# Kernel optimization log

Hardware: AMD Instinct MI355X
Metric: run time of the kernel (lower is better)

## Reference

```python
import jax, jax.numpy as jnp
import numpy as np

B, L, D, H = 4, 2048, 1024, 16
HD = D // H  # head_dim = 64


def setup_inputs() -> dict:
    key = jax.random.key(0)
    k1, k2, k3, k4 = jax.random.split(key, 4)
    x = jax.random.normal(k1, (B, L, D), dtype=jnp.float32)
    key_padding_mask = jax.random.randint(k2, (B, L), 0, 2) == 1
    scale = 1.0 / np.sqrt(D)
    Wqkv = jax.random.normal(k3, (3 * D, D), dtype=jnp.float32) * scale
    Wproj = jax.random.normal(k4, (D, D), dtype=jnp.float32) * scale
    return {"x": x, "key_padding_mask": key_padding_mask, "Wqkv": Wqkv, "Wproj": Wproj}


def reference(x, key_padding_mask, Wqkv, Wproj):
    b, l, d = x.shape
    qkv = jnp.einsum('bld,ed->ble', x, Wqkv)          # [B, L, 3D]
    q, k, v = jnp.split(qkv, 3, axis=-1)
    # [B, H, L, HD]
    q = q.reshape(b, l, H, HD).transpose(0, 2, 1, 3)
    k = k.reshape(b, l, H, HD).transpose(0, 2, 1, 3)
    v = v.reshape(b, l, H, HD).transpose(0, 2, 1, 3)
    scale = 1.0 / jnp.sqrt(jnp.asarray(HD, dtype=x.dtype))
    scores = jnp.einsum('bhqd,bhkd->bhqk', q, k) * scale  # [B, H, L, L]
    # key_padding_mask True = PAD -> -inf bias on key axis
    bias = jnp.where(key_padding_mask[:, None, None, :], -jnp.inf, 0.0).astype(x.dtype)
    attn = jax.nn.softmax(scores + bias, axis=-1)
    y = jnp.einsum('bhqk,bhkd->bhqd', attn, v)            # [B, H, L, HD]
    y = y.transpose(0, 2, 1, 3).reshape(b, l, d)          # [B, L, D]
    return jnp.einsum('bld,ed->ble', y, Wproj)
```

## Files before the change

kernel.cpp:

```cpp
#include <hip/hip_runtime.h>

#define L_SEQ 2048
#define DIM   1024
#define NH    16
#define HDIM  64
#define KDIM  1024

typedef short  short8 __attribute__((ext_vector_type(8)));
typedef __bf16 bf16x8 __attribute__((ext_vector_type(8)));
typedef __bf16 bf16x4 __attribute__((ext_vector_type(4)));
typedef float  f32x4  __attribute__((ext_vector_type(4)));
typedef unsigned u32x4 __attribute__((ext_vector_type(4)));

__device__ __forceinline__ unsigned short f2bf(float f) {
  unsigned u = __builtin_bit_cast(unsigned, f);
  u += 0x7fffu + ((u >> 16) & 1u);
  return (unsigned short)(u >> 16);
}

__device__ __forceinline__ void gload16(const void* g, void* l) {
  __builtin_amdgcn_global_load_lds(
      (const __attribute__((address_space(1))) void*)g,
      (__attribute__((address_space(3))) void*)l, 16, 0, 0);
}

__device__ __forceinline__ bf16x8 ldfrag(const unsigned short* p) {
  return __builtin_bit_cast(bf16x8, *(const short8*)p);
}
#define MFMA16(a, b, c) __builtin_amdgcn_mfma_f32_16x16x32_bf16(a, b, c, 0, 0, 0)

__device__ __forceinline__ unsigned cvtpk(float a, float b) {
  unsigned r;
  asm("v_cvt_pk_bf16_f32 %0, %1, %2" : "=v"(r) : "v"(a), "v"(b));
  return r;
}
__device__ __forceinline__ void xchg(unsigned &a, unsigned &b) {
  asm("v_permlane32_swap_b32 %0, %1" : "+v"(a), "+v"(b));
  asm("v_permlane16_swap_b32 %0, %1" : "+v"(a), "+v"(b));
}

__device__ __forceinline__ float foldmax_g(float v) {
  float y;
  asm("v_mov_b32 %0, %1" : "=&v"(y) : "v"(v));
  asm("v_permlane32_swap_b32 %0, %1" : "+v"(v), "+v"(y));
  v = fmaxf(v, y);
  float z;
  asm("v_mov_b32 %0, %1" : "=&v"(z) : "v"(v));
  asm("v_permlane16_swap_b32 %0, %1" : "+v"(v), "+v"(z));
  return fmaxf(v, z);
}

__device__ __forceinline__ void cvt_chunk(const float* __restrict__ src,
                                          unsigned short* __restrict__ dst,
                                          int blk, int t) {
  int i = (blk * 256 + t) * 8;
  f32x4 a = *(const f32x4*)(src + i);
  f32x4 b = *(const f32x4*)(src + i + 4);
  short8 o;
  o[0] = (short)f2bf(a[0]); o[1] = (short)f2bf(a[1]);
  o[2] = (short)f2bf(a[2]); o[3] = (short)f2bf(a[3]);
  o[4] = (short)f2bf(b[0]); o[5] = (short)f2bf(b[1]);
  o[6] = (short)f2bf(b[2]); o[7] = (short)f2bf(b[3]);
  *(short8*)(dst + i) = o;
}

__global__ __launch_bounds__(256) void prep(
    const float* __restrict__ x, const float* __restrict__ wqkv,
    const float* __restrict__ wproj, const int* __restrict__ mask,
    unsigned short* __restrict__ xb, unsigned short* __restrict__ wqkvb,
    unsigned short* __restrict__ wprojb,
    int* __restrict__ rowl, int* __restrict__ lc) {
  const int bid = blockIdx.x, t = threadIdx.x;
  if (bid < 4096)      { cvt_chunk(x,     xb,     bid,        t); return; }
  if (bid < 5632)      { cvt_chunk(wqkv,  wqkvb,  bid - 4096, t); return; }
  if (bid < 6144)      { cvt_chunk(wproj, wprojb, bid - 5632, t); return; }
  const int b = bid - 6144;
  __shared__ int wsum[4];
  __shared__ int lcs;
  const int* mrow = mask + b * L_SEQ + t * 8;
  int m[8], c = 0;
#pragma unroll
  for (int i = 0; i < 8; ++i) { m[i] = mrow[i]; c += (m[i] == 0); }
  const int lane = t & 63, w = t >> 6;
  int sc = c;
#pragma unroll
  for (int d = 1; d < 64; d <<= 1) {
    int v = __shfl_up(sc, d);
    if (lane >= d) sc += v;
  }
  if (lane == 63) wsum[w] = sc;
  __syncthreads();
  int pre = sc - c;
  for (int i = 0; i < w; ++i) pre += wsum[i];
  int run = pre;
#pragma unroll
  for (int i = 0; i < 8; ++i) {
    if (m[i] == 0) { rowl[b * L_SEQ + run] = t * 8 + i; ++run; }
  }
  if (t == 255) { lc[b] = run; lcs = run; }
  __syncthreads();
  int total = lcs;
#pragma unroll
  for (int i = 0; i < 8; ++i) {
    int slot = t * 8 + i;
    if (slot >= total) rowl[b * L_SEQ + slot] = 0;
  }
}

__device__ __forceinline__ void gemm512_mainloop(
    const unsigned short* __restrict__ A, const unsigned short* __restrict__ Bt,
    const int (&asrc)[2], int n0,
    unsigned short* As0, unsigned short* As1,
    unsigned short* Bs0, unsigned short* Bs1,
    f32x4 (&acc)[4][2]) {
  const int t = threadIdx.x;
  const int lane = t & 63, wid = t >> 6;
  const int wm = wid >> 2, wn = wid & 3;
  const int lr = lane & 15, lk = (lane >> 4) * 8;
  const int swr = (lr & 7) << 3;
  constexpr int NT = KDIM / 64;

  auto stage = [&](unsigned short* Ad, unsigned short* Bd, int kt) {
#pragma unroll
    for (int i = 0; i < 2; ++i) {
      int c = i * 512 + t;
      int row = c >> 3;
      int cs = ((c & 7) ^ (row & 7)) * 8;
      gload16(A + (size_t)asrc[i] * KDIM + kt * 64 + cs,
              Ad + row * 64 + (c & 7) * 8);
    }
#pragma unroll
    for (int i = 0; i < 2; ++i) {
      int c = i * 512 + t;
      int row = c >> 3;
      int cs = ((c & 7) ^ (row & 7)) * 8;
      gload16(Bt + (size_t)(n0 + row) * KDIM + kt * 64 + cs,
              Bd + row * 64 + (c & 7) * 8);
    }
  };

  auto tile = [&](const unsigned short* Ac, const unsigned short* Bc,
                  unsigned short* An, unsigned short* Bn, int kt) {
    if (kt + 1 < NT) {
      stage(An, Bn, kt + 1);
      asm volatile("s_waitcnt vmcnt(4)" ::: "memory");
    } else {
      asm volatile("s_waitcnt vmcnt(0)" ::: "memory");
    }
    __builtin_amdgcn_sched_barrier(0);
    __builtin_amdgcn_s_barrier();
    __builtin_amdgcn_sched_barrier(0);
    bf16x8 af[4][2], bfv[2][2];
#pragma unroll
    for (int mf = 0; mf < 4; ++mf)
#pragma unroll
      for (int kh = 0; kh < 2; ++kh)
        af[mf][kh] = ldfrag(Ac + (wm * 64 + mf * 16 + lr) * 64 +
                            ((kh * 32 + lk) ^ swr));
#pragma unroll
    for (int nf = 0; nf < 2; ++nf)
#pragma unroll
      for (int kh = 0; kh < 2; ++kh)
        bfv[nf][kh] = ldfrag(Bc + (wn * 32 + nf * 16 + lr) * 64 +
                             ((kh * 32 + lk) ^ swr));
    __builtin_amdgcn_s_setprio(1);
#pragma unroll
    for (int mf = 0; mf < 4; ++mf)
#pragma unroll
      for (int nf = 0; nf < 2; ++nf) {
        acc[mf][nf] = MFMA16(af[mf][0], bfv[nf][0], acc[mf][nf]);
        acc[mf][nf] = MFMA16(af[mf][1], bfv[nf][1], acc[mf][nf]);
      }
    __builtin_amdgcn_s_setprio(0);
    __builtin_amdgcn_sched_barrier(0);
    __builtin_amdgcn_s_barrier();
  };

  stage(As0, Bs0, 0);
  for (int kt = 0; kt < NT; kt += 2) {
    tile(As0, Bs0, As1, Bs1, kt);
    tile(As1, Bs1, As0, Bs0, kt + 1);
  }
}

__global__ __launch_bounds__(512, 4) void gemm_qkv(
    const unsigned short* __restrict__ xb, const unsigned short* __restrict__ wb,
    const int* __restrict__ rowl, const int* __restrict__ lc,
    unsigned short* __restrict__ qw, unsigned short* __restrict__ kw,
    unsigned short* __restrict__ vtw) {
  __shared__ unsigned short As[2][128 * 64];
  __shared__ unsigned short Bs[2][128 * 64];
  const int nx = blockIdx.x;
  const int m0 = blockIdx.y * 128;
  const int sec = nx >> 3;
  const int n0 = nx * 128;
  const int b = m0 >> 11;
  const int lcb = lc[b];
  if (sec > 0 && (m0 & 2047) >= lcb) return;
  const int t = threadIdx.x;
  int asrc[2];
#pragma unroll
  for (int i = 0; i < 2; ++i) {
    int p = m0 + i * 64 + (t >> 3);
    asrc[i] = (sec == 0) ? p : ((p & ~2047) + rowl[p]);
  }
  f32x4 acc[4][2] = {};
  gemm512_mainloop(xb, wb, asrc, n0, As[0], As[1], Bs[0], Bs[1], acc);

  const int lane = t & 63, wid = t >> 6;
  const int wm = wid >> 2, wn = wid & 3;
  const int lr = lane & 15, g4 = (lane >> 4) * 4;
  const int nb = n0 & 1023;
  if (sec == 0) {
#pragma unroll
    for (int mf = 0; mf < 4; ++mf)
#pragma unroll
      for (int nf = 0; nf < 2; ++nf) {
        int e2 = nb + wn * 32 + nf * 16 + lr;
        int h = e2 >> 6, hd = e2 & 63;
#pragma unroll
        for (int r = 0; r < 4; ++r) {
          int m = m0 + wm * 64 + mf * 16 + g4 + r;
          qw[(((size_t)(b * NH + h)) * L_SEQ + (m & 2047)) * HDIM + hd] =
              f2bf(acc[mf][nf][r]);
        }
      }
  } else {
#pragma unroll
    for (int mf = 0; mf < 4; ++mf)
#pragma unroll
      for (int r = 0; r < 4; ++r) {
        int m = m0 + wm * 64 + mf * 16 + g4 + r;
        int tgt = m & 2047;
        size_t bb = (size_t)b * NH;
        if (sec == 1) {
          if (tgt >= lcb) continue;
#pragma unroll
          for (int nf = 0; nf < 2; ++nf) {
            int e2 = nb + wn * 32 + nf * 16 + lr;
            int h = e2 >> 6, hd = e2 & 63;
            kw[((bb + h) * L_SEQ + tgt) * HDIM + hd] = f2bf(acc[mf][nf][r]);
          }
        } else {
#pragma unroll
          for (int nf = 0; nf < 2; ++nf) {
            int e2 = nb + wn * 32 + nf * 16 + lr;
            int h = e2 >> 6, hd = e2 & 63;
            unsigned short val = (tgt < lcb) ? f2bf(acc[mf][nf][r])
                                             : (unsigned short)0;
            vtw[((bb + h) * HDIM + hd) * L_SEQ + tgt] = val;
          }
        }
      }
  }
}

__global__ __launch_bounds__(512, 4) void gemm_proj(
    const unsigned short* __restrict__ yb, const unsigned short* __restrict__ wb,
    float* __restrict__ out) {
  __shared__ unsigned short As[2][128 * 64];
  __shared__ unsigned short Bs[2][128 * 64];
  const int n0 = blockIdx.x * 128, m0 = blockIdx.y * 128;
  const int t = threadIdx.x;
  int asrc[2];
#pragma unroll
  for (int i = 0; i < 2; ++i) asrc[i] = m0 + i * 64 + (t >> 3);
  f32x4 acc[4][2] = {};
  gemm512_mainloop(yb, wb, asrc, n0, As[0], As[1], Bs[0], Bs[1], acc);
  const int lane = t & 63, wid = t >> 6;
  const int wm = wid >> 2, wn = wid & 3;
  const int lr = lane & 15, g4 = (lane >> 4) * 4;
#pragma unroll
  for (int mf = 0; mf < 4; ++mf)
#pragma unroll
    for (int nf = 0; nf < 2; ++nf) {
      int e2 = n0 + wn * 32 + nf * 16 + lr;
#pragma unroll
      for (int r = 0; r < 4; ++r) {
        int m = m0 + wm * 64 + mf * 16 + g4 + r;
        out[(size_t)m * DIM + e2] = acc[mf][nf][r];
      }
    }
}

__global__ __launch_bounds__(256, 4) void attn_kernel(
    const unsigned short* __restrict__ qw, const unsigned short* __restrict__ kw,
    const unsigned short* __restrict__ vtw, const int* __restrict__ lc,
    unsigned short* __restrict__ yb) {
  __shared__ unsigned short Ks[2][64 * 64];
  __shared__ unsigned short Vts[2][64 * 64];
  const int bh = blockIdx.y;
  const int q0 = blockIdx.x * 128;
  const int b = bh >> 4, h = bh & 15;
  const int t = threadIdx.x, wid = t >> 6, lane = t & 63;
  const int lr = lane & 15, lk = (lane >> 4) * 8, g4 = (lane >> 4) * 4;
  const int swr = (lr & 7) << 3;
  const float KE = 0.18033688011112042f;

  const int Lcv = lc[b];
  const int nt = (Lcv + 63) >> 6;

  bf16x8 qf[2][2];
  const size_t qbase = (size_t)bh * L_SEQ + q0 + wid * 32;
#pragma unroll
  for (int qi = 0; qi < 2; ++qi)
#pragma unroll
    for (int kh = 0; kh < 2; ++kh)
      qf[qi][kh] = __builtin_bit_cast(bf16x8,
          *(const short8*)(qw + (qbase + qi * 16 + lr) * HDIM + kh * 32 + lk));

  f32x4 o[2][4] = {};
  float mrun[2] = {-3.0e38f, -3.0e38f};
  float lrun[2] = {0.f, 0.f};

  auto stage = [&](int buf, int kt) {
#pragma unroll
    for (int i = 0; i < 2; ++i) {
      int c = i * 256 + t;
      int row = c >> 3;
      int cs = ((c & 7) ^ (row & 7)) * 8;
      gload16(kw  + ((size_t)bh * L_SEQ + kt * 64 + row) * HDIM + cs, &Ks[buf][c * 8]);
      gload16(vtw + ((size_t)bh * HDIM + row) * L_SEQ + kt * 64 + cs, &Vts[buf][c * 8]);
    }
  };

  stage(0, 0);
  int cur = 0;

  for (int kt = 0; kt < nt; ++kt) {
    if (kt + 1 < nt) {
      stage(cur ^ 1, kt + 1);
      asm volatile("s_waitcnt vmcnt(4)" ::: "memory");
    } else {
      asm volatile("s_waitcnt vmcnt(0)" ::: "memory");
    }
    __builtin_amdgcn_s_barrier();
    __builtin_amdgcn_sched_barrier(0);

    const unsigned short* Kc = Ks[cur];
    f32x4 s[2][4] = {};
    __builtin_amdgcn_s_setprio(1);
#pragma unroll
    for (int nf = 0; nf < 4; ++nf) {
      bf16x8 k0 = __builtin_bit_cast(bf16x8,
          *(const short8*)(Kc + (nf * 16 + lr) * 64 + ((0 + lk) ^ swr)));
      bf16x8 k1 = __builtin_bit_cast(bf16x8,
          *(const short8*)(Kc + (nf * 16 + lr) * 64 + ((32 + lk) ^ swr)));
      s[0][nf] = MFMA16(k0, qf[0][0], s[0][nf]);
      s[0][nf] = MFMA16(k1, qf[0][1], s[0][nf]);
      s[1][nf] = MFMA16(k0, qf[1][0], s[1][nf]);
      s[1][nf] = MFMA16(k1, qf[1][1], s[1][nf]);
    }
    __builtin_amdgcn_s_setprio(0);

    if (kt == nt - 1) {
      int kbase = kt * 64 + g4;
#pragma unroll
      for (int nf = 0; nf < 4; ++nf)
#pragma unroll
        for (int r = 0; r < 4; ++r)
          if (kbase + nf * 16 + r >= Lcv) {
            s[0][nf][r] = -3.0e38f;
            s[1][nf][r] = -3.0e38f;
          }
    }

    float pmax[2];
#pragma unroll
    for (int qi = 0; qi < 2; ++qi) {
      float a0 = fmaxf(fmaxf(s[qi][0][0], s[qi][0][1]), fmaxf(s[qi][0][2], s[qi][0][3]));
      float a1 = fmaxf(fmaxf(s[qi][1][0], s[qi][1][1]), fmaxf(s[qi][1][2], s[qi][1][3]));
      float a2 = fmaxf(fmaxf(s[qi][2][0], s[qi][2][1]), fmaxf(s[qi][2][2], s[qi][2][3]));
      float a3 = fmaxf(fmaxf(s[qi][3][0], s[qi][3][1]), fmaxf(s[qi][3][2], s[qi][3][3]));
      pmax[qi] = foldmax_g(fmaxf(fmaxf(a0, a1), fmaxf(a2, a3)));
    }

    bool need = (pmax[0] > mrun[0] + 8.0f) || (pmax[1] > mrun[1] + 8.0f);
    if (__any(need)) {
#pragma unroll
      for (int qi = 0; qi < 2; ++qi) {
        float mn = fmaxf(mrun[qi], pmax[qi]);
        float al = __builtin_amdgcn_exp2f((mrun[qi] - mn) * KE);
        mrun[qi] = mn;
        lrun[qi] *= al;
#pragma unroll
        for (int df = 0; df < 4; ++df) o[qi][df] *= al;
      }
    }

    bf16x8 pb[2][2];
#pragma unroll
    for (int qi = 0; qi < 2; ++qi) {
      float mk_ = mrun[qi] * KE;
      f32x4 rs4 = {0.f, 0.f, 0.f, 0.f};
#pragma unroll
      for (int nf = 0; nf < 4; ++nf) {
#pragma unroll
        for (int r = 0; r < 4; ++r)
          s[qi][nf][r] = __builtin_amdgcn_exp2f(s[qi][nf][r] * KE - mk_);
        rs4 += s[qi][nf];
      }
      lrun[qi] += (rs4[0] + rs4[1]) + (rs4[2] + rs4[3]);
      unsigned w00 = cvtpk(s[qi][0][0], s[qi][0][1]);
      unsigned w01 = cvtpk(s[qi][0][2], s[qi][0][3]);
      unsigned w10 = cvtpk(s[qi][1][0], s[qi][1][1]);
      unsigned w11 = cvtpk(s[qi][1][2], s[qi][1][3]);
      unsigned w20 = cvtpk(s[qi][2][0], s[qi][2][1]);
      unsigned w21 = cvtpk(s[qi][2][2], s[qi][2][3]);
      unsigned w30 = cvtpk(s[qi][3][0], s[qi][3][1]);
      unsigned w31 = cvtpk(s[qi][3][2], s[qi][3][3]);
      xchg(w00, w10);
      xchg(w01, w11);
      xchg(w20, w30);
      xchg(w21, w31);
      u32x4 f0 = {w00, w01, w10, w11};
      u32x4 f1 = {w20, w21, w30, w31};
      pb[qi][0] = __builtin_bit_cast(bf16x8, f0);
      pb[qi][1] = __builtin_bit_cast(bf16x8, f1);
    }

    const unsigned short* Vc = Vts[cur];
    __builtin_amdgcn_s_setprio(1);
#pragma unroll
    for (int df = 0; df < 4; ++df) {
      bf16x8 v0 = __builtin_bit_cast(bf16x8,
          *(const short8*)(Vc + (df * 16 + lr) * 64 + ((0 + lk) ^ swr)));
      bf16x8 v1 = __builtin_bit_cast(bf16x8,
          *(const short8*)(Vc + (df * 16 + lr) * 64 + ((32 + lk) ^ swr)));
      o[0][df] = MFMA16(v0, pb[0][0], o[0][df]);
      o[0][df] = MFMA16(v1, pb[0][1], o[0][df]);
      o[1][df] = MFMA16(v0, pb[1][0], o[1][df]);
      o[1][df] = MFMA16(v1, pb[1][1], o[1][df]);
    }
    __builtin_amdgcn_s_setprio(0);

    __builtin_amdgcn_sched_barrier(0);
    __builtin_amdgcn_s_barrier();
    cur ^= 1;
  }

#pragma unroll
  for (int qi = 0; qi < 2; ++qi) {
    float tot = lrun[qi];
    tot += __shfl_xor(tot, 16);
    tot += __shfl_xor(tot, 32);
    float inv = 1.0f / tot;
    int q = q0 + wid * 32 + qi * 16 + lr;
#pragma unroll
    for (int df = 0; df < 4; ++df) {
      bf16x4 pk = {(__bf16)(o[qi][df][0] * inv), (__bf16)(o[qi][df][1] * inv),
                   (__bf16)(o[qi][df][2] * inv), (__bf16)(o[qi][df][3] * inv)};
      *(bf16x4*)(yb + ((size_t)b * L_SEQ + q) * DIM + h * 64 + df * 16 + g4) = pk;
    }
  }
}

extern "C" void kernel_launch(void* const* d_in, const int* in_sizes, int n_in,
                              void* d_out, int out_size, void* d_ws, size_t ws_size,
                              hipStream_t stream) {
  const float* x     = (const float*)d_in[0];
  const int*   mask  = (const int*)d_in[1];
  const float* wqkv  = (const float*)d_in[2];
  const float* wproj = (const float*)d_in[3];
  char* ws = (char*)d_ws;
  unsigned short* xb     = (unsigned short*)(ws + 0);
  unsigned short* wqkvb  = (unsigned short*)(ws + 16777216);
  unsigned short* wprojb = (unsigned short*)(ws + 23068672);
  unsigned short* qw     = (unsigned short*)(ws + 25165824);
  unsigned short* kw     = (unsigned short*)(ws + 41943040);
  unsigned short* vtw    = (unsigned short*)(ws + 58720256);
  unsigned short* yb     = (unsigned short*)(ws + 75497472);
  int*            rowl   = (int*)(ws + 92274688);
  int*            lcArr  = (int*)(ws + 92307456);

  prep<<<dim3(6148), 256, 0, stream>>>(x, wqkv, wproj, mask,
                                       xb, wqkvb, wprojb, rowl, lcArr);
  gemm_qkv<<<dim3(24, 64), 512, 0, stream>>>(xb, wqkvb, rowl, lcArr, qw, kw, vtw);
  attn_kernel<<<dim3(16, 64), 256, 0, stream>>>(qw, kw, vtw, lcArr, yb);
  gemm_proj<<<dim3(8, 64), 512, 0, stream>>>(yb, wprojb, (float*)d_out);
}
```

Baseline: 156.7 us.

## Split attention work across 8 waves with 16 query rows each

The attention block now runs 512 threads (8 waves), and each wave owns 16 query rows instead of 32. The K/V staging is spread over more threads, so each thread issues one load pair per tile and the wait count drops to match. This halves per-thread accumulator and score registers and doubles the waves available to hide latency, so more waves share each staged K/V tile. The cost is that each wave does half as many MFMAs per K/V fragment read from shared memory, which raises the LDS traffic per FLOP, and the barriers now synchronise more waves.

Measured after the change: 159.0 us. About the same (+1.5%).

```diff
diff --git a/kernel.cpp b/kernel.cpp
--- a/kernel.cpp
+++ b/kernel.cpp
@@ -283,7 +283,7 @@
     }
 }
 
-__global__ __launch_bounds__(256, 4) void attn_kernel(
+__global__ __launch_bounds__(512, 8) void attn_kernel(
     const unsigned short* __restrict__ qw, const unsigned short* __restrict__ kw,
     const unsigned short* __restrict__ vtw, const int* __restrict__ lc,
     unsigned short* __restrict__ yb) {
@@ -300,28 +300,24 @@
   const int Lcv = lc[b];
   const int nt = (Lcv + 63) >> 6;
 
-  bf16x8 qf[2][2];
-  const size_t qbase = (size_t)bh * L_SEQ + q0 + wid * 32;
-#pragma unroll
-  for (int qi = 0; qi < 2; ++qi)
-#pragma unroll
-    for (int kh = 0; kh < 2; ++kh)
-      qf[qi][kh] = __builtin_bit_cast(bf16x8,
-          *(const short8*)(qw + (qbase + qi * 16 + lr) * HDIM + kh * 32 + lk));
-
-  f32x4 o[2][4] = {};
-  float mrun[2] = {-3.0e38f, -3.0e38f};
-  float lrun[2] = {0.f, 0.f};
+  bf16x8 qf[2];
+  const size_t qrow = (size_t)bh * L_SEQ + q0 + wid * 16 + lr;
+#pragma unroll
+  for (int kh = 0; kh < 2; ++kh)
+    qf[kh] = __builtin_bit_cast(bf16x8,
+        *(const short8*)(qw + qrow * HDIM + kh * 32 + lk));
+
+  f32x4 o[4] = {};
+  float mrun = -3.0e38f;
+  float lrun = 0.f;
 
   auto stage = [&](int buf, int kt) {
-#pragma unroll
-    for (int i = 0; i < 2; ++i) {
-      int c = i * 256 + t;
-      int row = c >> 3;
-      int cs = ((c & 7) ^ (row & 7)) * 8;
-      gload16(kw  + ((size_t)bh * L_SEQ + kt * 64 + row) * HDIM + cs, &Ks[buf][c * 8]);
-      gload16(vtw + ((size_t)bh * HDIM + row) * L_SEQ + kt * 64 + cs, &Vts[buf][c * 8]);
-    }
+    int row = t >> 3;
+    int cs = ((t & 7) ^ (row & 7)) * 8;
+    gload16(kw  + ((size_t)bh * L_SEQ + kt * 64 + row) * HDIM + cs,
+            &Ks[buf][t * 8]);
+    gload16(vtw + ((size_t)bh * HDIM + row) * L_SEQ + kt * 64 + cs,
+            &Vts[buf][t * 8]);
   };
 
   stage(0, 0);
@@ -330,7 +326,7 @@
   for (int kt = 0; kt < nt; ++kt) {
     if (kt + 1 < nt) {
       stage(cur ^ 1, kt + 1);
-      asm volatile("s_waitcnt vmcnt(4)" ::: "memory");
+      asm volatile("s_waitcnt vmcnt(2)" ::: "memory");
     } else {
       asm volatile("s_waitcnt vmcnt(0)" ::: "memory");
     }
@@ -338,7 +334,7 @@
     __builtin_amdgcn_sched_barrier(0);
 
     const unsigned short* Kc = Ks[cur];
-    f32x4 s[2][4] = {};
+    f32x4 s[4] = {};
     __builtin_amdgcn_s_setprio(1);
 #pragma unroll
     for (int nf = 0; nf < 4; ++nf) {
@@ -346,10 +342,8 @@
           *(const short8*)(Kc + (nf * 16 + lr) * 64 + ((0 + lk) ^ swr)));
       bf16x8 k1 = __builtin_bit_cast(bf16x8,
           *(const short8*)(Kc + (nf * 16 + lr) * 64 + ((32 + lk) ^ swr)));
-      s[0][nf] = MFMA16(k0, qf[0][0], s[0][nf]);
-      s[0][nf] = MFMA16(k1, qf[0][1], s[0][nf]);
-      s[1][nf] = MFMA16(k0, qf[1][0], s[1][nf]);
-      s[1][nf] = MFMA16(k1, qf[1][1], s[1][nf]);
+      s[nf] = MFMA16(k0, qf[0], s[nf]);
+      s[nf] = MFMA16(k1, qf[1], s[nf]);
     }
     __builtin_amdgcn_s_setprio(0);
 
@@ -359,65 +353,50 @@
       for (int nf = 0; nf < 4; ++nf)
 #pragma unroll
         for (int r = 0; r < 4; ++r)
-          if (kbase + nf * 16 + r >= Lcv) {
-            s[0][nf][r] = -3.0e38f;
-            s[1][nf][r] = -3.0e38f;
-          }
-    }
-
-    float pmax[2];
-#pragma unroll
-    for (int qi = 0; qi < 2; ++qi) {
-      float a0 = fmaxf(fmaxf(s[qi][0][0], s[qi][0][1]), fmaxf(s[qi][0][2], s[qi][0][3]));
-      float a1 = fmaxf(fmaxf(s[qi][1][0], s[qi][1][1]), fmaxf(s[qi][1][2], s[qi][1][3]));
-      float a2 = fmaxf(fmaxf(s[qi][2][0], s[qi][2][1]), fmaxf(s[qi][2][2], s[qi][2][3]));
-      float a3 = fmaxf(fmaxf(s[qi][3][0], s[qi][3][1]), fmaxf(s[qi][3][2], s[qi][3][3]));
-      pmax[qi] = foldmax_g(fmaxf(fmaxf(a0, a1), fmaxf(a2, a3)));
-    }
-
-    bool need = (pmax[0] > mrun[0] + 8.0f) || (pmax[1] > mrun[1] + 8.0f);
-    if (__any(need)) {
-#pragma unroll
-      for (int qi = 0; qi < 2; ++qi) {
-        float mn = fmaxf(mrun[qi], pmax[qi]);
-        float al = __builtin_amdgcn_exp2f((mrun[qi] - mn) * KE);
-        mrun[qi] = mn;
-        lrun[qi] *= al;
-#pragma unroll
-        for (int df = 0; df < 4; ++df) o[qi][df] *= al;
-      }
-    }
-
-    bf16x8 pb[2][2];
-#pragma unroll
-    for (int qi = 0; qi < 2; ++qi) {
-      float mk_ = mrun[qi] * KE;
-      f32x4 rs4 = {0.f, 0.f, 0.f, 0.f};
-#pragma unroll
-      for (int nf = 0; nf < 4; ++nf) {
-#pragma unroll
-        for (int r = 0; r < 4; ++r)
-          s[qi][nf][r] = __builtin_amdgcn_exp2f(s[qi][nf][r] * KE - mk_);
-        rs4 += s[qi][nf];
-      }
-      lrun[qi] += (rs4[0] + rs4[1]) + (rs4[2] + rs4[3]);
-      unsigned w00 = cvtpk(s[qi][0][0], s[qi][0][1]);
-      unsigned w01 = cvtpk(s[qi][0][2], s[qi][0][3]);
-      unsigned w10 = cvtpk(s[qi][1][0], s[qi][1][1]);
-      unsigned w11 = cvtpk(s[qi][1][2], s[qi][1][3]);
-      unsigned w20 = cvtpk(s[qi][2][0], s[qi][2][1]);
-      unsigned w21 = cvtpk(s[qi][2][2], s[qi][2][3]);
-      unsigned w30 = cvtpk(s[qi][3][0], s[qi][3][1]);
-      unsigned w31 = cvtpk(s[qi][3][2], s[qi][3][3]);
-      xchg(w00, w10);
-      xchg(w01, w11);
-      xchg(w20, w30);
-      xchg(w21, w31);
-      u32x4 f0 = {w00, w01, w10, w11};
-      u32x4 f1 = {w20, w21, w30, w31};
-      pb[qi][0] = __builtin_bit_cast(bf16x8, f0);
-      pb[qi][1] = __builtin_bit_cast(bf16x8, f1);
-    }
+          if (kbase + nf * 16 + r >= Lcv) s[nf][r] = -3.0e38f;
+    }
+
+    float a0 = fmaxf(fmaxf(s[0][0], s[0][1]), fmaxf(s[0][2], s[0][3]));
+    float a1 = fmaxf(fmaxf(s[1][0], s[1][1]), fmaxf(s[1][2], s[1][3]));
+    float a2 = fmaxf(fmaxf(s[2][0], s[2][1]), fmaxf(s[2][2], s[2][3]));
+    float a3 = fmaxf(fmaxf(s[3][0], s[3][1]), fmaxf(s[3][2], s[3][3]));
+    float pmax = foldmax_g(fmaxf(fmaxf(a0, a1), fmaxf(a2, a3)));
+
+    if (__any(pmax > mrun + 8.0f)) {
+      float mn = fmaxf(mrun, pmax);
+      float al = __builtin_amdgcn_exp2f((mrun - mn) * KE);
+      mrun = mn;
+      lrun *= al;
+#pragma unroll
+      for (int df = 0; df < 4; ++df) o[df] *= al;
+    }
+
+    float mk_ = mrun * KE;
+    f32x4 rs4 = {0.f, 0.f, 0.f, 0.f};
+#pragma unroll
+    for (int nf = 0; nf < 4; ++nf) {
+#pragma unroll
+      for (int r = 0; r < 4; ++r)
+        s[nf][r] = __builtin_amdgcn_exp2f(s[nf][r] * KE - mk_);
+      rs4 += s[nf];
+    }
+    lrun += (rs4[0] + rs4[1]) + (rs4[2] + rs4[3]);
+    unsigned w00 = cvtpk(s[0][0], s[0][1]);
+    unsigned w01 = cvtpk(s[0][2], s[0][3]);
+    unsigned w10 = cvtpk(s[1][0], s[1][1]);
+    unsigned w11 = cvtpk(s[1][2], s[1][3]);
+    unsigned w20 = cvtpk(s[2][0], s[2][1]);
+    unsigned w21 = cvtpk(s[2][2], s[2][3]);
+    unsigned w30 = cvtpk(s[3][0], s[3][1]);
+    unsigned w31 = cvtpk(s[3][2], s[3][3]);
+    xchg(w00, w10);
+    xchg(w01, w11);
+    xchg(w20, w30);
+    xchg(w21, w31);
+    u32x4 f0 = {w00, w01, w10, w11};
+    u32x4 f1 = {w20, w21, w30, w31};
+    bf16x8 pb0 = __builtin_bit_cast(bf16x8, f0);
+    bf16x8 pb1 = __builtin_bit_cast(bf16x8, f1);
 
     const unsigned short* Vc = Vts[cur];
     __builtin_amdgcn_s_setprio(1);
@@ -427,10 +406,8 @@
           *(const short8*)(Vc + (df * 16 + lr) * 64 + ((0 + lk) ^ swr)));
       bf16x8 v1 = __builtin_bit_cast(bf16x8,
           *(const short8*)(Vc + (df * 16 + lr) * 64 + ((32 + lk) ^ swr)));
-      o[0][df] = MFMA16(v0, pb[0][0], o[0][df]);
-      o[0][df] = MFMA16(v1, pb[0][1], o[0][df]);
-      o[1][df] = MFMA16(v0, pb[1][0], o[1][df]);
-      o[1][df] = MFMA16(v1, pb[1][1], o[1][df]);
+      o[df] = MFMA16(v0, pb0, o[df]);
+      o[df] = MFMA16(v1, pb1, o[df]);
     }
     __builtin_amdgcn_s_setprio(0);
 
@@ -439,19 +416,16 @@
     cur ^= 1;
   }
 
-#pragma unroll
-  for (int qi = 0; qi < 2; ++qi) {
-    float tot = lrun[qi];
-    tot += __shfl_xor(tot, 16);
-    tot += __shfl_xor(tot, 32);
-    float inv = 1.0f / tot;
-    int q = q0 + wid * 32 + qi * 16 + lr;
-#pragma unroll
-    for (int df = 0; df < 4; ++df) {
-      bf16x4 pk = {(__bf16)(o[qi][df][0] * inv), (__bf16)(o[qi][df][1] * inv),
-                   (__bf16)(o[qi][df][2] * inv), (__bf16)(o[qi][df][3] * inv)};
-      *(bf16x4*)(yb + ((size_t)b * L_SEQ + q) * DIM + h * 64 + df * 16 + g4) = pk;
-    }
+  float tot = lrun;
+  tot += __shfl_xor(tot, 16);
+  tot += __shfl_xor(tot, 32);
+  float inv = 1.0f / tot;
+  int q = q0 + wid * 16 + lr;
+#pragma unroll
+  for (int df = 0; df < 4; ++df) {
+    bf16x4 pk = {(__bf16)(o[df][0] * inv), (__bf16)(o[df][1] * inv),
+                 (__bf16)(o[df][2] * inv), (__bf16)(o[df][3] * inv)};
+    *(bf16x4*)(yb + ((size_t)b * L_SEQ + q) * DIM + h * 64 + df * 16 + g4) = pk;
   }
 }
 
@@ -476,6 +450,6 @@
   prep<<<dim3(6148), 256, 0, stream>>>(x, wqkv, wproj, mask,
                                        xb, wqkvb, wprojb, rowl, lcArr);
   gemm_qkv<<<dim3(24, 64), 512, 0, stream>>>(xb, wqkvb, rowl, lcArr, qw, kw, vtw);
-  attn_kernel<<<dim3(16, 64), 256, 0, stream>>>(qw, kw, vtw, lcArr, yb);
+  attn_kernel<<<dim3(16, 64), 512, 0, stream>>>(qw, kw, vtw, lcArr, yb);
   gemm_proj<<<dim3(8, 64), 512, 0, stream>>>(yb, wprojb, (float*)d_out);
 }
```
